# Kernel tuning notes

Hardware: AMD Instinct MI355X
Metric: run time of the kernel (lower is better)

## Reference

```python
import jax, jax.numpy as jnp
import numpy as np

DIM = 1024
H = 16
HEAD_DIM = 64
HIDDEN = H * HEAD_DIM  # == DIM, required by the module's reshape
SCALE = HEAD_DIM ** -0.5


def setup_inputs() -> dict:
    key = jax.random.key(0)
    k_x, k_qkv, k_w1, k_b1 = jax.random.split(key, 4)
    B, N = 8, 1024
    x = jax.random.normal(k_x, (B, N, DIM), dtype=jnp.float32)
    # nn.Linear stores weight as [out, in]; we keep [in, out] for x @ W
    w_qkv = jax.random.normal(k_qkv, (DIM, 3 * HIDDEN), dtype=jnp.float32) * (DIM ** -0.5)
    w_out = jax.random.normal(k_w1, (HIDDEN, DIM), dtype=jnp.float32) * (HIDDEN ** -0.5)
    b_out = jax.random.normal(k_b1, (DIM,), dtype=jnp.float32) * 0.02
    return {"x": x, "w_qkv": w_qkv, "w_out": w_out, "b_out": b_out}


def reference(x, w_qkv, w_out, b_out):
    B, N, C = x.shape
    # QKV projection (no bias), split into heads
    qkv = (x @ w_qkv).reshape(B, N, 3, H, C // H)
    q, k, v = qkv[:, :, 0], qkv[:, :, 1], qkv[:, :, 2]  # [B, N, H, d]
    attn = jnp.einsum("bqhd,bkhd->bhqk", q, k) * SCALE
    attn = jax.nn.softmax(attn, axis=-1)  # dropout inactive at eval
    out = jnp.einsum("bhqk,bkhd->bqhd", attn, v).reshape(B, N, C)
    return out @ w_out + b_out
```

## Files before the change

kernel.cpp:

```cpp
#include <hip/hip_runtime.h>
#include <hip/hip_bf16.h>

#define B_SZ 8
#define SEQ 1024
#define DIM_ 1024
#define NH 16
#define HD 64
#define M_TOT (B_SZ*SEQ)
#define N_QKV (3*DIM_)

typedef __attribute__((ext_vector_type(8))) short bf16x8;
typedef __attribute__((ext_vector_type(4))) float f32x4;

typedef const __attribute__((address_space(1))) void gvoid;
typedef __attribute__((address_space(3))) void lvoid;

__device__ __forceinline__ short f2bf(float f){
  union { __hip_bfloat16 h; short s; } u;
  u.h = __float2bfloat16(f);
  return u.s;
}

__global__ void cvt_kernel(const float* __restrict__ in, short* __restrict__ out, int n4){
  int i = blockIdx.x*blockDim.x + threadIdx.x;
  int stride = gridDim.x*blockDim.x;
  for (; i < n4; i += stride){
    float4 v = reinterpret_cast<const float4*>(in)[i];
    short4 s;
    s.x = f2bf(v.x); s.y = f2bf(v.y); s.z = f2bf(v.z); s.w = f2bf(v.w);
    reinterpret_cast<short4*>(out)[i] = s;
  }
}

__global__ void tconv_kernel(const float* __restrict__ in, short* __restrict__ out, int R, int C){
  __shared__ alignas(16) short tile[64][66];
  const int l = threadIdx.x & 63, w = threadIdx.x >> 6;
  const int r0 = blockIdx.y * 64, c0 = blockIdx.x * 64;
  #pragma unroll
  for (int rr = 0; rr < 16; ++rr){
    int r = w + rr*4;
    tile[r][l] = f2bf(in[(size_t)(r0+r)*C + c0 + l]);
  }
  __syncthreads();
  #pragma unroll
  for (int cc = 0; cc < 16; ++cc){
    int c = w + cc*4;
    out[(size_t)(c0+c)*R + r0 + l] = tile[l][c];
  }
}

template<int EPI, int GX, int NOFF>
__global__ __launch_bounds__(256, 4) void gemm5(
    const short* __restrict__ A, const short* __restrict__ Bt,
    int M, int Nn, int K,
    short* __restrict__ Qb, short* __restrict__ Kb, short* __restrict__ Vtb,
    const float* __restrict__ bias, float* __restrict__ outF)
{
  __shared__ alignas(16) short As[2][128*32];
  __shared__ alignas(16) short Bs[2][128*32];

  const int orig = blockIdx.x;
  const int xcd = orig & 7, t = orig >> 3;
  const int by = xcd*8 + t/GX, bx = t % GX;

  const int tid = threadIdx.x;
  const int l = tid & 63, wid = tid >> 6;
  const int wr = wid >> 1, wc = wid & 1;
  const int lr = l & 15, lw = l >> 4;
  const int sw = (lr >> 1) & 3;
  const int m0 = by * 128, n0 = (bx + NOFF) * 128;

  f32x4 acc[4][4];
  const f32x4 zz = {0.f,0.f,0.f,0.f};
  #pragma unroll
  for (int m=0;m<4;m++)
    #pragma unroll
    for (int n=0;n<4;n++) acc[m][n] = zz;

  auto STAGE = [&](int buf, int kt){
    const int k0 = kt << 5;
    #pragma unroll
    for (int j=0;j<2;j++){
      const int idx = j*256 + tid;
      const int row = idx >> 2;
      const int ws  = (idx & 3) ^ ((row >> 1) & 3);
      __builtin_amdgcn_global_load_lds(
          (gvoid*)(A + (size_t)(m0+row)*K + k0 + ws*8),
          (lvoid*)(&As[buf][idx*8]), 16, 0, 0);
    }
    #pragma unroll
    for (int j=0;j<2;j++){
      const int idx = j*256 + tid;
      const int row = idx >> 2;
      const int ws  = (idx & 3) ^ ((row >> 1) & 3);
      __builtin_amdgcn_global_load_lds(
          (gvoid*)(Bt + (size_t)(n0+row)*K + k0 + ws*8),
          (lvoid*)(&Bs[buf][idx*8]), 16, 0, 0);
    }
  };

  STAGE(0, 0);
  __syncthreads();

  const int NT = K >> 5;
  int buf = 0;
  for (int kt = 0; kt < NT; ++kt){
    if (kt + 1 < NT) STAGE(buf ^ 1, kt + 1);

    bf16x8 af[4], bfr[4];
    const int wsel = (lw ^ sw) << 3;
    #pragma unroll
    for (int m=0;m<4;m++){
      const int r = wr*64 + m*16 + lr;
      af[m] = *(const bf16x8*)(&As[buf][r*32 + wsel]);
    }
    #pragma unroll
    for (int n=0;n<4;n++){
      const int r = wc*64 + n*16 + lr;
      bfr[n] = *(const bf16x8*)(&Bs[buf][r*32 + wsel]);
    }
    #pragma unroll
    for (int m=0;m<4;m++)
      #pragma unroll
      for (int n=0;n<4;n++)
        acc[m][n] = __builtin_amdgcn_mfma_f32_16x16x32_bf16(af[m], bfr[n], acc[m][n], 0, 0, 0);

    __syncthreads();
    buf ^= 1;
  }

  #pragma unroll
  for (int n=0;n<4;n++){
    const int col = n0 + wc*64 + n*16 + lr;
    if (EPI == 0){
      const int three = col >> 10;
      const int cc = col & 1023;
      const int h = cc >> 6, d = cc & 63;
      #pragma unroll
      for (int m=0;m<4;m++){
        const int rbase = m0 + wr*64 + m*16 + (lw<<2);
        const int b = rbase >> 10, nn = rbase & 1023;
        const int bh = b*NH + h;
        if (three == 2){
          short4 pk;
          pk.x = f2bf(acc[m][n][0]); pk.y = f2bf(acc[m][n][1]);
          pk.z = f2bf(acc[m][n][2]); pk.w = f2bf(acc[m][n][3]);
          *(short4*)(&Vtb[((size_t)bh*HD + d)*SEQ + nn]) = pk;
        } else if (three == 0){
          #pragma unroll
          for (int ri=0;ri<4;ri++)
            Qb[((size_t)bh*SEQ + nn + ri)*HD + d] = f2bf(acc[m][n][ri] * 0.1803368801f);
        } else {
          #pragma unroll
          for (int ri=0;ri<4;ri++)
            Kb[((size_t)bh*SEQ + nn + ri)*HD + d] = f2bf(acc[m][n][ri]);
        }
      }
    } else {
      const float bv = bias[col];
      #pragma unroll
      for (int m=0;m<4;m++){
        const int rbase = m0 + wr*64 + m*16 + (lw<<2);
        #pragma unroll
        for (int ri=0;ri<4;ri++)
          outF[(size_t)(rbase+ri)*Nn + col] = acc[m][n][ri] + bv;
      }
    }
  }
}

__global__ __launch_bounds__(256) void attn_kernel(
    const short* __restrict__ Q, const short* __restrict__ Kb,
    const short* __restrict__ Vt, short* __restrict__ Ao)
{
  __shared__ alignas(16) short Ks[2][64*64];
  __shared__ alignas(16) short Vs[2][64*64];
  __shared__ alignas(16) short Ps[4][16*72];

  const int tid = threadIdx.x;
  const int l = tid & 63, w = tid >> 6;
  const int bid = blockIdx.x;
  const int qt = bid & 15, bh = bid >> 4;
  const int b = bh >> 4, h = bh & 15;
  const size_t base = (size_t)bh << 16;

  const int lr = l & 15;
  const int q4 = l >> 4;
  const int lk = q4 << 3;
  const int sw8 = lr & 7;

  const int qrow = qt*64 + w*16 + lr;
  const short* qp = Q + base + (size_t)qrow*HD + lk;
  const bf16x8 qf0 = *(const bf16x8*)qp;
  const bf16x8 qf1 = *(const bf16x8*)(qp + 32);

  float m_run = -1e30f, l_run = 0.f;
  f32x4 o[4];
  #pragma unroll
  for (int i=0;i<4;i++) o[i] = f32x4{0.f,0.f,0.f,0.f};

  bf16x8 kr[2], vr[2];
  auto load_tile = [&](int kt){
    const int kv0 = kt*64;
    #pragma unroll
    for (int p=0;p<2;p++){
      const int idx = tid + p*256;
      const int row = idx >> 3, c8 = (idx & 7) << 3;
      kr[p] = *(const bf16x8*)(Kb + base + (size_t)(kv0+row)*HD + c8);
      vr[p] = *(const bf16x8*)(Vt + base + (size_t)row*SEQ + kv0 + c8);
    }
  };
  auto write_tile = [&](int bi){
    #pragma unroll
    for (int p=0;p<2;p++){
      const int idx = tid + p*256;
      const int row = idx >> 3;
      const int wsw = ((idx & 7) ^ (row & 7)) << 3;
      *(bf16x8*)(&Ks[bi][row*64 + wsw]) = kr[p];
      *(bf16x8*)(&Vs[bi][row*64 + wsw]) = vr[p];
    }
  };

  load_tile(0);
  write_tile(0);
  __syncthreads();

  int cur = 0;
  for (int kt = 0; kt < 16; ++kt){
    if (kt < 15) load_tile(kt+1);

    const short* kb = &Ks[cur][0];
    const short* vb = &Vs[cur][0];

    f32x4 s[4];
    #pragma unroll
    for (int cg=0;cg<4;cg++) s[cg] = f32x4{0.f,0.f,0.f,0.f};
    __builtin_amdgcn_s_setprio(1);
    #pragma unroll
    for (int cg=0;cg<4;cg++){
      const short* kp = kb + (cg*16 + lr)*64;
      bf16x8 kf0 = *(const bf16x8*)(kp + ((q4     ^ sw8) << 3));
      bf16x8 kf1 = *(const bf16x8*)(kp + (((q4+4) ^ sw8) << 3));
      s[cg] = __builtin_amdgcn_mfma_f32_16x16x32_bf16(kf0, qf0, s[cg], 0,0,0);
      s[cg] = __builtin_amdgcn_mfma_f32_16x16x32_bf16(kf1, qf1, s[cg], 0,0,0);
    }
    __builtin_amdgcn_s_setprio(0);

    float mt = s[0][0];
    #pragma unroll
    for (int cg=0;cg<4;cg++)
      #pragma unroll
      for (int ri=0;ri<4;ri++) mt = fmaxf(mt, s[cg][ri]);
    mt = fmaxf(mt, __shfl_xor(mt, 16));
    mt = fmaxf(mt, __shfl_xor(mt, 32));

    const float mn = fmaxf(m_run, mt);
    const float corr = __builtin_amdgcn_exp2f(m_run - mn);
    m_run = mn;

    float p[4][4], rs = 0.f;
    #pragma unroll
    for (int cg=0;cg<4;cg++)
      #pragma unroll
      for (int ri=0;ri<4;ri++){
        p[cg][ri] = __builtin_amdgcn_exp2f(s[cg][ri] - mn);
        rs += p[cg][ri];
      }
    rs += __shfl_xor(rs, 16);
    rs += __shfl_xor(rs, 32);
    l_run = l_run*corr + rs;

    short* pw = &Ps[w][0];
    #pragma unroll
    for (int cg=0;cg<4;cg++){
      short4 pk;
      pk.x = f2bf(p[cg][0]); pk.y = f2bf(p[cg][1]);
      pk.z = f2bf(p[cg][2]); pk.w = f2bf(p[cg][3]);
      *(short4*)(pw + lr*72 + cg*16 + q4*4) = pk;
    }

    float corr_r[4];
    #pragma unroll
    for (int ri=0;ri<4;ri++) corr_r[ri] = __shfl(corr, (q4<<2) + ri);
    #pragma unroll
    for (int dg=0;dg<4;dg++)
      #pragma unroll
      for (int ri=0;ri<4;ri++) o[dg][ri] *= corr_r[ri];

    const bf16x8 pa0 = *(const bf16x8*)(pw + lr*72 + lk);
    const bf16x8 pa1 = *(const bf16x8*)(pw + lr*72 + lk + 32);
    __builtin_amdgcn_s_setprio(1);
    #pragma unroll
    for (int dg=0;dg<4;dg++){
      const short* vp = vb + (dg*16 + lr)*64;
      bf16x8 vf0 = *(const bf16x8*)(vp + ((q4     ^ sw8) << 3));
      bf16x8 vf1 = *(const bf16x8*)(vp + (((q4+4) ^ sw8) << 3));
      o[dg] = __builtin_amdgcn_mfma_f32_16x16x32_bf16(pa0, vf0, o[dg], 0,0,0);
      o[dg] = __builtin_amdgcn_mfma_f32_16x16x32_bf16(pa1, vf1, o[dg], 0,0,0);
    }
    __builtin_amdgcn_s_setprio(0);

    if (kt < 15) write_tile(cur ^ 1);
    __syncthreads();
    cur ^= 1;
  }

  float linv[4];
  #pragma unroll
  for (int ri=0;ri<4;ri++) linv[ri] = 1.0f / __shfl(l_run, (q4<<2) + ri);
  #pragma unroll
  for (int ri=0;ri<4;ri++){
    const int row = qt*64 + w*16 + (q4<<2) + ri;
    short* op = Ao + ((size_t)(b*SEQ + row))*DIM_ + h*HD;
    #pragma unroll
    for (int dg=0;dg<4;dg++)
      op[dg*16 + lr] = f2bf(o[dg][ri] * linv[ri]);
  }
}

extern "C" void kernel_launch(void* const* d_in, const int* in_sizes, int n_in,
                              void* d_out, int out_size, void* d_ws, size_t ws_size,
                              hipStream_t stream)
{
  (void)in_sizes; (void)n_in; (void)out_size; (void)ws_size;
  const float* x     = (const float*)d_in[0];
  const float* w_qkv = (const float*)d_in[1];
  const float* w_out = (const float*)d_in[2];
  const float* b_out = (const float*)d_in[3];
  float* out = (float*)d_out;

  char* ws = (char*)d_ws;
  const size_t MB = (size_t)1 << 20;
  short* xb    = (short*)(ws);
  short* wqkvT = (short*)(ws + 16*MB);
  short* woutT = (short*)(ws + 22*MB);
  short* Qb    = (short*)(ws + 24*MB);
  short* Kb    = (short*)(ws + 40*MB);
  short* Vtb   = (short*)(ws + 56*MB);
  short* Aob   = (short*)(ws + 72*MB);

  cvt_kernel<<<2048, 256, 0, stream>>>(x, xb, (M_TOT*DIM_)/4);
  tconv_kernel<<<dim3(N_QKV/64, DIM_/64), 256, 0, stream>>>(w_qkv, wqkvT, DIM_, N_QKV);
  tconv_kernel<<<dim3(DIM_/64, DIM_/64), 256, 0, stream>>>(w_out, woutT, DIM_, DIM_);

  gemm5<0,16,0><<<1024, 256, 0, stream>>>(
      xb, wqkvT, M_TOT, N_QKV, DIM_, Qb, Kb, Vtb, nullptr, nullptr);

  gemm5<0,8,16><<<512, 256, 0, stream>>>(
      xb, wqkvT, M_TOT, N_QKV, DIM_, Qb, Kb, Vtb, nullptr, nullptr);

  attn_kernel<<<B_SZ*NH*(SEQ/64), 256, 0, stream>>>(Qb, Kb, Vtb, Aob);

  gemm5<1,8,0><<<512, 256, 0, stream>>>(
      Aob, woutT, M_TOT, DIM_, DIM_, nullptr, nullptr, nullptr, b_out, out);
}
```

Baseline: 191.1 us.

## Double query rows per attention block, use direct global-to-LDS loads, XCD-aware mapping

Each warp in the attention kernel now handles two 16-row query tiles instead of one, so each 64-row query block becomes 128 rows. Every K/V tile staged in LDS is reused for twice as many queries, and the grid shrinks from 2048 to 1024 blocks. K/V staging now goes through global_load_lds straight into swizzled LDS, removing the register round trip. Block indices are also remapped so that blocks of the same batch-head land on the same XCD for L2 locality. The cost is higher register pressure and fewer blocks, which may reduce occupancy.

```diff
diff --git a/kernel.cpp b/kernel.cpp
--- a/kernel.cpp
+++ b/kernel.cpp
@@ -175,12 +175,14 @@
 {
   __shared__ alignas(16) short Ks[2][64*64];
   __shared__ alignas(16) short Vs[2][64*64];
-  __shared__ alignas(16) short Ps[4][16*72];
+  __shared__ alignas(16) short Ps[4][32*72];
 
   const int tid = threadIdx.x;
   const int l = tid & 63, w = tid >> 6;
-  const int bid = blockIdx.x;
-  const int qt = bid & 15, bh = bid >> 4;
+  const int orig = blockIdx.x;
+  const int xcd = orig & 7, n_ = orig >> 3;
+  const int g = n_ >> 3, qt = n_ & 7;
+  const int bh = g*8 + xcd;
   const int b = bh >> 4, h = bh & 15;
   const size_t base = (size_t)bh << 16;
 
@@ -189,132 +191,168 @@
   const int lk = q4 << 3;
   const int sw8 = lr & 7;
 
-  const int qrow = qt*64 + w*16 + lr;
-  const short* qp = Q + base + (size_t)qrow*HD + lk;
-  const bf16x8 qf0 = *(const bf16x8*)qp;
-  const bf16x8 qf1 = *(const bf16x8*)(qp + 32);
-
-  float m_run = -1e30f, l_run = 0.f;
-  f32x4 o[4];
-  #pragma unroll
-  for (int i=0;i<4;i++) o[i] = f32x4{0.f,0.f,0.f,0.f};
-
-  bf16x8 kr[2], vr[2];
-  auto load_tile = [&](int kt){
+  const int qrowA = qt*128 + w*32 + lr;
+  const short* qpA = Q + base + (size_t)qrowA*HD + lk;
+  const bf16x8 qfA0 = *(const bf16x8*)qpA;
+  const bf16x8 qfA1 = *(const bf16x8*)(qpA + 32);
+  const short* qpB = qpA + 16*HD;
+  const bf16x8 qfB0 = *(const bf16x8*)qpB;
+  const bf16x8 qfB1 = *(const bf16x8*)(qpB + 32);
+
+  float mA = -1e30f, lA = 0.f, mB = -1e30f, lB = 0.f;
+  f32x4 oA[4], oB[4];
+  #pragma unroll
+  for (int i=0;i<4;i++){ oA[i] = f32x4{0.f,0.f,0.f,0.f}; oB[i] = f32x4{0.f,0.f,0.f,0.f}; }
+
+  auto STAGE = [&](int bi, int kt){
     const int kv0 = kt*64;
     #pragma unroll
-    for (int p=0;p<2;p++){
-      const int idx = tid + p*256;
-      const int row = idx >> 3, c8 = (idx & 7) << 3;
-      kr[p] = *(const bf16x8*)(Kb + base + (size_t)(kv0+row)*HD + c8);
-      vr[p] = *(const bf16x8*)(Vt + base + (size_t)row*SEQ + kv0 + c8);
+    for (int j=0;j<2;j++){
+      const int idx = j*256 + tid;
+      const int row = idx >> 3;
+      const int wsw = (idx & 7) ^ (row & 7);
+      __builtin_amdgcn_global_load_lds(
+          (gvoid*)(Kb + base + (size_t)(kv0+row)*HD + wsw*8),
+          (lvoid*)(&Ks[bi][idx*8]), 16, 0, 0);
+      __builtin_amdgcn_global_load_lds(
+          (gvoid*)(Vt + base + (size_t)row*SEQ + kv0 + wsw*8),
+          (lvoid*)(&Vs[bi][idx*8]), 16, 0, 0);
     }
   };
-  auto write_tile = [&](int bi){
-    #pragma unroll
-    for (int p=0;p<2;p++){
-      const int idx = tid + p*256;
-      const int row = idx >> 3;
-      const int wsw = ((idx & 7) ^ (row & 7)) << 3;
-      *(bf16x8*)(&Ks[bi][row*64 + wsw]) = kr[p];
-      *(bf16x8*)(&Vs[bi][row*64 + wsw]) = vr[p];
-    }
-  };
-
-  load_tile(0);
-  write_tile(0);
+
+  STAGE(0, 0);
   __syncthreads();
 
   int cur = 0;
   for (int kt = 0; kt < 16; ++kt){
-    if (kt < 15) load_tile(kt+1);
+    if (kt < 15) STAGE(cur ^ 1, kt+1);
 
     const short* kb = &Ks[cur][0];
     const short* vb = &Vs[cur][0];
 
-    f32x4 s[4];
-    #pragma unroll
-    for (int cg=0;cg<4;cg++) s[cg] = f32x4{0.f,0.f,0.f,0.f};
+    f32x4 sA[4], sB[4];
+    #pragma unroll
+    for (int cg=0;cg<4;cg++){ sA[cg] = f32x4{0.f,0.f,0.f,0.f}; sB[cg] = f32x4{0.f,0.f,0.f,0.f}; }
     __builtin_amdgcn_s_setprio(1);
     #pragma unroll
     for (int cg=0;cg<4;cg++){
       const short* kp = kb + (cg*16 + lr)*64;
       bf16x8 kf0 = *(const bf16x8*)(kp + ((q4     ^ sw8) << 3));
       bf16x8 kf1 = *(const bf16x8*)(kp + (((q4+4) ^ sw8) << 3));
-      s[cg] = __builtin_amdgcn_mfma_f32_16x16x32_bf16(kf0, qf0, s[cg], 0,0,0);
-      s[cg] = __builtin_amdgcn_mfma_f32_16x16x32_bf16(kf1, qf1, s[cg], 0,0,0);
+      sA[cg] = __builtin_amdgcn_mfma_f32_16x16x32_bf16(kf0, qfA0, sA[cg], 0,0,0);
+      sA[cg] = __builtin_amdgcn_mfma_f32_16x16x32_bf16(kf1, qfA1, sA[cg], 0,0,0);
+      sB[cg] = __builtin_amdgcn_mfma_f32_16x16x32_bf16(kf0, qfB0, sB[cg], 0,0,0);
+      sB[cg] = __builtin_amdgcn_mfma_f32_16x16x32_bf16(kf1, qfB1, sB[cg], 0,0,0);
     }
     __builtin_amdgcn_s_setprio(0);
 
-    float mt = s[0][0];
-    #pragma unroll
-    for (int cg=0;cg<4;cg++)
-      #pragma unroll
-      for (int ri=0;ri<4;ri++) mt = fmaxf(mt, s[cg][ri]);
-    mt = fmaxf(mt, __shfl_xor(mt, 16));
-    mt = fmaxf(mt, __shfl_xor(mt, 32));
-
-    const float mn = fmaxf(m_run, mt);
-    const float corr = __builtin_amdgcn_exp2f(m_run - mn);
-    m_run = mn;
-
-    float p[4][4], rs = 0.f;
-    #pragma unroll
-    for (int cg=0;cg<4;cg++)
-      #pragma unroll
-      for (int ri=0;ri<4;ri++){
-        p[cg][ri] = __builtin_amdgcn_exp2f(s[cg][ri] - mn);
-        rs += p[cg][ri];
+    short* pw = &Ps[w][0];
+
+    {
+      float mt = sA[0][0];
+      #pragma unroll
+      for (int cg=0;cg<4;cg++)
+        #pragma unroll
+        for (int ri=0;ri<4;ri++) mt = fmaxf(mt, sA[cg][ri]);
+      mt = fmaxf(mt, __shfl_xor(mt, 16));
+      mt = fmaxf(mt, __shfl_xor(mt, 32));
+      const float mn = fmaxf(mA, mt);
+      const float corr = __builtin_amdgcn_exp2f(mA - mn);
+      mA = mn;
+      float rs = 0.f;
+      #pragma unroll
+      for (int cg=0;cg<4;cg++){
+        float p0 = __builtin_amdgcn_exp2f(sA[cg][0] - mn);
+        float p1 = __builtin_amdgcn_exp2f(sA[cg][1] - mn);
+        float p2 = __builtin_amdgcn_exp2f(sA[cg][2] - mn);
+        float p3 = __builtin_amdgcn_exp2f(sA[cg][3] - mn);
+        rs += (p0+p1)+(p2+p3);
+        short4 pk; pk.x=f2bf(p0); pk.y=f2bf(p1); pk.z=f2bf(p2); pk.w=f2bf(p3);
+        *(short4*)(pw + lr*72 + cg*16 + q4*4) = pk;
       }
-    rs += __shfl_xor(rs, 16);
-    rs += __shfl_xor(rs, 32);
-    l_run = l_run*corr + rs;
-
-    short* pw = &Ps[w][0];
-    #pragma unroll
-    for (int cg=0;cg<4;cg++){
-      short4 pk;
-      pk.x = f2bf(p[cg][0]); pk.y = f2bf(p[cg][1]);
-      pk.z = f2bf(p[cg][2]); pk.w = f2bf(p[cg][3]);
-      *(short4*)(pw + lr*72 + cg*16 + q4*4) = pk;
-    }
-
-    float corr_r[4];
-    #pragma unroll
-    for (int ri=0;ri<4;ri++) corr_r[ri] = __shfl(corr, (q4<<2) + ri);
-    #pragma unroll
-    for (int dg=0;dg<4;dg++)
-      #pragma unroll
-      for (int ri=0;ri<4;ri++) o[dg][ri] *= corr_r[ri];
-
-    const bf16x8 pa0 = *(const bf16x8*)(pw + lr*72 + lk);
-    const bf16x8 pa1 = *(const bf16x8*)(pw + lr*72 + lk + 32);
+      rs += __shfl_xor(rs, 16);
+      rs += __shfl_xor(rs, 32);
+      lA = lA*corr + rs;
+      float corr_r[4];
+      #pragma unroll
+      for (int ri=0;ri<4;ri++) corr_r[ri] = __shfl(corr, (q4<<2) + ri);
+      #pragma unroll
+      for (int dg=0;dg<4;dg++)
+        #pragma unroll
+        for (int ri=0;ri<4;ri++) oA[dg][ri] *= corr_r[ri];
+    }
+    {
+      float mt = sB[0][0];
+      #pragma unroll
+      for (int cg=0;cg<4;cg++)
+        #pragma unroll
+        for (int ri=0;ri<4;ri++) mt = fmaxf(mt, sB[cg][ri]);
+      mt = fmaxf(mt, __shfl_xor(mt, 16));
+      mt = fmaxf(mt, __shfl_xor(mt, 32));
+      const float mn = fmaxf(mB, mt);
+      const float corr = __builtin_amdgcn_exp2f(mB - mn);
+      mB = mn;
+      float rs = 0.f;
+      #pragma unroll
+      for (int cg=0;cg<4;cg++){
+        float p0 = __builtin_amdgcn_exp2f(sB[cg][0] - mn);
+        float p1 = __builtin_amdgcn_exp2f(sB[cg][1] - mn);
+        float p2 = __builtin_amdgcn_exp2f(sB[cg][2] - mn);
+        float p3 = __builtin_amdgcn_exp2f(sB[cg][3] - mn);
+        rs += (p0+p1)+(p2+p3);
+        short4 pk; pk.x=f2bf(p0); pk.y=f2bf(p1); pk.z=f2bf(p2); pk.w=f2bf(p3);
+        *(short4*)(pw + (16+lr)*72 + cg*16 + q4*4) = pk;
+      }
+      rs += __shfl_xor(rs, 16);
+      rs += __shfl_xor(rs, 32);
+      lB = lB*corr + rs;
+      float corr_r[4];
+      #pragma unroll
+      for (int ri=0;ri<4;ri++) corr_r[ri] = __shfl(corr, (q4<<2) + ri);
+      #pragma unroll
+      for (int dg=0;dg<4;dg++)
+        #pragma unroll
+        for (int ri=0;ri<4;ri++) oB[dg][ri] *= corr_r[ri];
+    }
+
+    const bf16x8 paA0 = *(const bf16x8*)(pw + lr*72 + lk);
+    const bf16x8 paA1 = *(const bf16x8*)(pw + lr*72 + lk + 32);
+    const bf16x8 paB0 = *(const bf16x8*)(pw + (16+lr)*72 + lk);
+    const bf16x8 paB1 = *(const bf16x8*)(pw + (16+lr)*72 + lk + 32);
+
     __builtin_amdgcn_s_setprio(1);
     #pragma unroll
     for (int dg=0;dg<4;dg++){
       const short* vp = vb + (dg*16 + lr)*64;
       bf16x8 vf0 = *(const bf16x8*)(vp + ((q4     ^ sw8) << 3));
       bf16x8 vf1 = *(const bf16x8*)(vp + (((q4+4) ^ sw8) << 3));
-      o[dg] = __builtin_amdgcn_mfma_f32_16x16x32_bf16(pa0, vf0, o[dg], 0,0,0);
-      o[dg] = __builtin_amdgcn_mfma_f32_16x16x32_bf16(pa1, vf1, o[dg], 0,0,0);
+      oA[dg] = __builtin_amdgcn_mfma_f32_16x16x32_bf16(paA0, vf0, oA[dg], 0,0,0);
+      oA[dg] = __builtin_amdgcn_mfma_f32_16x16x32_bf16(paA1, vf1, oA[dg], 0,0,0);
+      oB[dg] = __builtin_amdgcn_mfma_f32_16x16x32_bf16(paB0, vf0, oB[dg], 0,0,0);
+      oB[dg] = __builtin_amdgcn_mfma_f32_16x16x32_bf16(paB1, vf1, oB[dg], 0,0,0);
     }
     __builtin_amdgcn_s_setprio(0);
 
-    if (kt < 15) write_tile(cur ^ 1);
     __syncthreads();
     cur ^= 1;
   }
 
-  float linv[4];
-  #pragma unroll
-  for (int ri=0;ri<4;ri++) linv[ri] = 1.0f / __shfl(l_run, (q4<<2) + ri);
+  float linvA[4], linvB[4];
   #pragma unroll
   for (int ri=0;ri<4;ri++){
-    const int row = qt*64 + w*16 + (q4<<2) + ri;
-    short* op = Ao + ((size_t)(b*SEQ + row))*DIM_ + h*HD;
-    #pragma unroll
-    for (int dg=0;dg<4;dg++)
-      op[dg*16 + lr] = f2bf(o[dg][ri] * linv[ri]);
+    linvA[ri] = 1.0f / __shfl(lA, (q4<<2) + ri);
+    linvB[ri] = 1.0f / __shfl(lB, (q4<<2) + ri);
+  }
+  #pragma unroll
+  for (int ri=0;ri<4;ri++){
+    const int rowA = qt*128 + w*32 + (q4<<2) + ri;
+    short* opA = Ao + ((size_t)(b*SEQ + rowA))*DIM_ + h*HD;
+    short* opB = opA + 16*DIM_;
+    #pragma unroll
+    for (int dg=0;dg<4;dg++){
+      opA[dg*16 + lr] = f2bf(oA[dg][ri] * linvA[ri]);
+      opB[dg*16 + lr] = f2bf(oB[dg][ri] * linvB[ri]);
+    }
   }
 }
 
@@ -349,7 +387,7 @@
   gemm5<0,8,16><<<512, 256, 0, stream>>>(
       xb, wqkvT, M_TOT, N_QKV, DIM_, Qb, Kb, Vtb, nullptr, nullptr);
 
-  attn_kernel<<<B_SZ*NH*(SEQ/64), 256, 0, stream>>>(Qb, Kb, Vtb, Aob);
+  attn_kernel<<<1024, 256, 0, stream>>>(Qb, Kb, Vtb, Aob);
 
   gemm5<1,8,0><<<512, 256, 0, stream>>>(
       Aob, woutT, M_TOT, DIM_, DIM_, nullptr, nullptr, nullptr, b_out, out);
```

Measured after the change: 184.5 us. 1.04x faster.
